# Kernel tuning notes

Measured on AMD Instinct MI355X. Metric: run time of the kernel, lower is better.

## Reference

```python
import jax, jax.numpy as jnp
import numpy as np

B = 2
S0, S1, S2 = 1024, 256, 64
S = S0 + S1 + S2
H, KV, D = 16, 8, 128
H_VLM, H_EXP = 2048, 1024
F_VLM, F_EXP = 8192, 4096
EPS = 1e-6
ROPE_BASE = 1000000.0


def setup_inputs() -> dict:
    key = jax.random.key(0)
    ks = iter(jax.random.split(key, 64))

    def n(shape, scale=0.02):
        return jax.random.normal(next(ks), shape, jnp.float32) * scale

    inp = {}
    inp["x0"] = jax.random.normal(next(ks), (B, S0, H_VLM), jnp.float32)
    inp["x1"] = jax.random.normal(next(ks), (B, S1, H_EXP), jnp.float32)
    inp["x2"] = jax.random.normal(next(ks), (B, S2, H_EXP), jnp.float32)
    inp["attention_mask"] = jnp.zeros((B, 1, S, S), jnp.float32)
    inp["position_ids"] = jnp.broadcast_to(jnp.arange(S, dtype=jnp.int32), (B, S))
    for i, (hid, ffn) in enumerate([(H_VLM, F_VLM), (H_EXP, F_EXP), (H_EXP, F_EXP)]):
        p = f"e{i}_"
        inp[p + "ln1"] = jnp.ones((hid,), jnp.float32)
        inp[p + "ln2"] = jnp.ones((hid,), jnp.float32)
        inp[p + "wq"] = n((H * D, hid))
        inp[p + "wk"] = n((KV * D, hid))
        inp[p + "wv"] = n((KV * D, hid))
        inp[p + "wo"] = n((hid, H * D))
        inp[p + "qn"] = jnp.ones((D,), jnp.float32)
        inp[p + "kn"] = jnp.ones((D,), jnp.float32)
        inp[p + "wg"] = n((ffn, hid))
        inp[p + "wu"] = n((ffn, hid))
        inp[p + "wd"] = n((hid, ffn))
    return inp


def _rms(x, w):
    # Qwen3 RMSNorm (eps 1e-6), applied over the last dim
    return x * jax.lax.rsqrt(jnp.mean(x * x, axis=-1, keepdims=True) + EPS) * w


def _rope_cos_sin(pos):
    inv = 1.0 / (ROPE_BASE ** (jnp.arange(0, D, 2, dtype=jnp.float32) / D))
    freqs = pos.astype(jnp.float32)[..., None] * inv  # [B,S,D/2]
    emb = jnp.concatenate([freqs, freqs], axis=-1)  # [B,S,D]
    return jnp.cos(emb), jnp.sin(emb)


def _rot_half(x):
    x1, x2 = jnp.split(x, 2, axis=-1)
    return jnp.concatenate([-x2, x1], axis=-1)


def _forward(xs, params, attention_mask, position_ids):
    # Per-expert QKV projections with per-head q/k RMSNorm
    qs, ks, vs = [], [], []
    for x, p in zip(xs, params):
        ln1, ln2, wq, wk, wv, wo, qn, kn, wg, wu, wd = p
        h = _rms(x, ln1)
        b, s, _ = x.shape
        q = _rms(jnp.einsum('bsd,od->bso', h, wq).reshape(b, s, H, D), qn)
        k = _rms(jnp.einsum('bsd,od->bso', h, wk).reshape(b, s, KV, D), kn)
        v = jnp.einsum('bsd,od->bso', h, wv).reshape(b, s, KV, D)
        qs.append(q.transpose(0, 2, 1, 3))  # [B,H,s,D]
        ks.append(k.transpose(0, 2, 1, 3))
        vs.append(v.transpose(0, 2, 1, 3))
    # Joint cross-expert attention over concatenated sequence
    q = jnp.concatenate(qs, axis=2)  # [B,H,S,D]
    k = jnp.concatenate(ks, axis=2)  # [B,KV,S,D]
    v = jnp.concatenate(vs, axis=2)
    cos, sin = _rope_cos_sin(position_ids)
    cos, sin = cos[:, None], sin[:, None]  # unsqueeze head dim
    q = q * cos + _rot_half(q) * sin
    k = k * cos + _rot_half(k) * sin
    k = jnp.repeat(k, H // KV, axis=1)  # GQA repeat_kv
    v = jnp.repeat(v, H // KV, axis=1)
    scores = jnp.einsum('bhqd,bhkd->bhqk', q, k) * (D ** -0.5) + attention_mask
    probs = jax.nn.softmax(scores, axis=-1)
    att = jnp.einsum('bhqk,bhkd->bhqd', probs, v)
    att = att.transpose(0, 2, 1, 3).reshape(q.shape[0], -1, H * D)  # [B,S,H*D]
    # Split back per expert: o_proj + residual + post-LN + SwiGLU MLP + residual
    outs, start = [], 0
    for x, p in zip(xs, params):
        ln1, ln2, wq, wk, wv, wo, qn, kn, wg, wu, wd = p
        s = x.shape[1]
        o = jnp.einsum('bsi,oi->bso', att[:, start:start + s], wo) + x
        h = _rms(o, ln2)
        m = jax.nn.silu(jnp.einsum('bsd,fd->bsf', h, wg)) * jnp.einsum('bsd,fd->bsf', h, wu)
        outs.append(jnp.einsum('bsf,df->bsd', m, wd) + o)
        start += s
    return tuple(outs)


def reference(x0, x1, x2, attention_mask, position_ids,
              e0_ln1, e0_ln2, e0_wq, e0_wk, e0_wv, e0_wo, e0_qn, e0_kn, e0_wg, e0_wu, e0_wd,
              e1_ln1, e1_ln2, e1_wq, e1_wk, e1_wv, e1_wo, e1_qn, e1_kn, e1_wg, e1_wu, e1_wd,
              e2_ln1, e2_ln2, e2_wq, e2_wk, e2_wv, e2_wo, e2_qn, e2_kn, e2_wg, e2_wu, e2_wd):
    params = [
        (e0_ln1, e0_ln2, e0_wq, e0_wk, e0_wv, e0_wo, e0_qn, e0_kn, e0_wg, e0_wu, e0_wd),
        (e1_ln1, e1_ln2, e1_wq, e1_wk, e1_wv, e1_wo, e1_qn, e1_kn, e1_wg, e1_wu, e1_wd),
        (e2_ln1, e2_ln2, e2_wq, e2_wk, e2_wv, e2_wo, e2_qn, e2_kn, e2_wg, e2_wu, e2_wd),
    ]
    return _forward([x0, x1, x2], params, attention_mask, position_ids)
```

## Files before the change

### kernel.cpp

```cpp
#include <hip/hip_runtime.h>
#include <cstdint>
#include <cstddef>


using u16 = unsigned short;
typedef __attribute__((ext_vector_type(4))) float  f32x4;
typedef __attribute__((ext_vector_type(4))) u16    u16x4;
typedef __attribute__((ext_vector_type(8))) u16    u16x8;
typedef __attribute__((ext_vector_type(8))) short  s16x8;

__device__ __forceinline__ u16 f2bf(float f) {
  unsigned u = __builtin_bit_cast(unsigned, f);
  u = (u + 0x7FFF + ((u >> 16) & 1)) >> 16;
  return (u16)u;
}
__device__ __forceinline__ float bf2f(u16 h) {
  unsigned u = ((unsigned)h) << 16;
  return __builtin_bit_cast(float, u);
}
__device__ __forceinline__ f32x4 mfma16(s16x8 a, s16x8 b, f32x4 c) {
  return __builtin_amdgcn_mfma_f32_16x16x32_bf16(a, b, c, 0, 0, 0);
}
__device__ __forceinline__ void gl_lds16(const u16* g, u16* l) {
  __builtin_amdgcn_global_load_lds(
      (const __attribute__((address_space(1))) unsigned int*)g,
      (__attribute__((address_space(3))) unsigned int*)l, 16, 0, 0);
}

static constexpr size_t WB_OFF   = 0;
static constexpr size_t H1_OFF   = WB_OFF   + 201326592;
static constexpr size_t H2_OFF   = H1_OFF   + 9699328;
static constexpr size_t QKV_OFF  = H2_OFF   + 9699328;
static constexpr size_t QB_OFF   = QKV_OFF  + 22020096;
static constexpr size_t KB_OFF   = QB_OFF   + 11010048;
static constexpr size_t VT_OFF   = KB_OFF   + 5505024;
static constexpr size_t ATTO_OFF = VT_OFF   + 5505024;
static constexpr size_t GU_OFF   = ATTO_OFF + 11010048;
static constexpr size_t WS_NEED  = GU_OFF   + 77594624;

struct CastTab { const float* src[15]; int pre[16]; };
struct DstoArg { size_t v[15]; };

__global__ __launch_bounds__(256) void cast_weights2(CastTab tab, DstoArg dsto,
                                                     u16* __restrict__ dst) {
  int c = blockIdx.x;
  int a = 0;
  while (c >= tab.pre[a + 1]) a++;
  const f32x4* s = (const f32x4*)(tab.src[a] + ((size_t)(c - tab.pre[a]) << 15));
  u16x4* d = (u16x4*)(dst + dsto.v[a] + (((size_t)(c - tab.pre[a])) << 15));
  int t = threadIdx.x;
  for (int i = t; i < 8192; i += 256) {
    f32x4 v = s[i];
    u16x4 o; o[0] = f2bf(v[0]); o[1] = f2bf(v[1]); o[2] = f2bf(v[2]); o[3] = f2bf(v[3]);
    d[i] = o;
  }
}

__global__ __launch_bounds__(256) void cast_gu_all(
    const float* __restrict__ g0, const float* __restrict__ u0,
    const float* __restrict__ g1, const float* __restrict__ u1,
    const float* __restrict__ g2, const float* __restrict__ u2,
    u16* __restrict__ dst, size_t o0, size_t o1, size_t o2) {
  const long N0 = 8388608, N1 = 10485760, N2 = 12582912;
  long i = (long)blockIdx.x * 256 + threadIdx.x;
  long stride = (long)gridDim.x * 256;
  for (; i < N2; i += stride) {
    const float* g; const float* u; u16* d; int logh; long li;
    if (i < N0)      { g = g0; u = u0; d = dst + o0; logh = 11; li = i; }
    else if (i < N1) { g = g1; u = u1; d = dst + o1; logh = 10; li = i - N0; }
    else             { g = g2; u = u2; d = dst + o2; logh = 10; li = i - N1; }
    int hid = 1 << logh;
    long e4 = li << 2;
    long r = e4 >> logh;
    int  k = (int)(e4 & (hid - 1));
    long super = r >> 6; int sub = (int)(r & 63);
    const float* src = (sub < 32 ? g + ((super << 5) + sub) * (long)hid
                                 : u + ((super << 5) + (sub - 32)) * (long)hid) + k;
    f32x4 v = *(const f32x4*)src;
    u16x4 o; o[0] = f2bf(v[0]); o[1] = f2bf(v[1]); o[2] = f2bf(v[2]); o[3] = f2bf(v[3]);
    ((u16x4*)d)[li] = o;
  }
}

__global__ __launch_bounds__(256) void rms_all(
    const float* __restrict__ i0, const float* __restrict__ i1, const float* __restrict__ i2,
    const float* __restrict__ w0, const float* __restrict__ w1, const float* __restrict__ w2,
    u16* __restrict__ out) {
  int row = blockIdx.x;
  const float* xr; const float* wr; size_t oo; int hid;
  if (row < 2048)      { xr = i0 + (size_t)row * 2048; wr = w0; oo = (size_t)row * 2048; hid = 2048; }
  else if (row < 2560) { int r = row - 2048; xr = i1 + (size_t)r * 1024; wr = w1;
                         oo = 4194304 + (size_t)r * 1024; hid = 1024; }
  else                 { int r = row - 2560; xr = i2 + (size_t)r * 1024; wr = w2;
                         oo = 4718592 + (size_t)r * 1024; hid = 1024; }
  const f32x4* x4 = (const f32x4*)xr;
  const f32x4* w4 = (const f32x4*)wr;
  int n4 = hid >> 2;
  int t = threadIdx.x;
  float ss = 0.f;
  for (int i = t; i < n4; i += 256) {
    f32x4 v = x4[i];
    ss += v[0] * v[0] + v[1] * v[1] + v[2] * v[2] + v[3] * v[3];
  }
#pragma unroll
  for (int m = 1; m < 64; m <<= 1) ss += __shfl_xor(ss, m);
  __shared__ float part[4];
  if ((t & 63) == 0) part[t >> 6] = ss;
  __syncthreads();
  float tot = part[0] + part[1] + part[2] + part[3];
  float rs = rsqrtf(tot / (float)hid + 1e-6f);
  u16x4* orow = (u16x4*)(out + oo);
  for (int i = t; i < n4; i += 256) {
    f32x4 v = x4[i];
    f32x4 g = w4[i];
    u16x4 o;
    o[0] = f2bf(v[0] * rs * g[0]); o[1] = f2bf(v[1] * rs * g[1]);
    o[2] = f2bf(v[2] * rs * g[2]); o[3] = f2bf(v[3] * rs * g[3]);
    orow[i] = o;
  }
}

template <int MB, int N0>
__device__ __forceinline__ void mmblk(f32x4 (&acc)[8][4], const s16x8 (&afr)[2][4],
                                      const s16x8 (&bfr)[2][4]) {
#pragma unroll
  for (int ks = 0; ks < 2; ks++)
#pragma unroll
    for (int j = 0; j < 4; j++)
#pragma unroll
      for (int ni = 0; ni < 2; ni++)
        acc[MB + j][N0 + ni] =
            mfma16(afr[ks][j], bfr[ks][N0 + ni], acc[MB + j][N0 + ni]);
}

#define GB256_BAR() do { __builtin_amdgcn_sched_barrier(0); \
                         __builtin_amdgcn_s_barrier(); } while (0)
#define GB256_LGKM0() do { asm volatile("s_waitcnt lgkmcnt(0)" ::: "memory"); \
                           __builtin_amdgcn_sched_barrier(0); } while (0)

template <int RESID, int OUTBF, bool SPLIT, bool SILU>
__global__ __launch_bounds__(512, 2) void gemm256(
    const u16* __restrict__ A, int Astride, int logSe, int bstride, int rowoff,
    const u16* __restrict__ Bw, int K, int kLen, int N,
    void* __restrict__ C, const float* __restrict__ R, size_t mn) {
  __shared__ u16 As[256 * 64];
  __shared__ u16 Bs[256 * 64];
  const int t = threadIdx.x;

  int gx = gridDim.x, nwg = gx * gridDim.y;
  int flat = blockIdx.y * gx + blockIdx.x;
  int q = nwg >> 3, r8 = nwg & 7;
  int xcd = flat & 7, idx = flat >> 3;
  int nf = (xcd < r8 ? xcd * (q + 1) : r8 * (q + 1) + (xcd - r8) * q) + idx;
  const int nt = (nf % gx) * 256, mt = (nf / gx) * 256;

  const int w = t >> 6, l = t & 63;
  const int wm = (w >> 2) * 128, wn = (w & 3) * 64;
  const int l15 = l & 15, lg = l >> 4;
  const int sr8 = t >> 3, u8 = t & 7;
  const int mask_se = (1 << logSe) - 1;
  const int k0 = SPLIT ? (int)blockIdx.z * kLen : 0;
  const int kLast = k0 + kLen - 64;

  f32x4 acc[8][4];
#pragma unroll
  for (int i = 0; i < 8; i++)
#pragma unroll
    for (int j = 0; j < 4; j++) acc[i][j] = (f32x4){0.f, 0.f, 0.f, 0.f};

  auto stA = [&](int qb, int ktv) {
    int row = qb + sr8;
    int gr = mt + row;
    int grow = ((gr >> logSe) * bstride) + (gr & mask_se) + rowoff;
    int su = u8 ^ (row & 7);
    gl_lds16(A + (size_t)grow * Astride + ktv + su * 8, &As[row * 64 + u8 * 8]);
  };
  auto stB = [&](int half, int pair, int ktv) {
    int row = (pair * 2 + (t >> 8)) * 64 + half * 32 + ((t & 255) >> 3);
    int su = u8 ^ (row & 7);
    gl_lds16(Bw + (size_t)(nt + row) * K + ktv + su * 8, &Bs[row * 64 + u8 * 8]);
  };
  auto rdA = [&](int mi, int ks) -> s16x8 {
    int row = wm + mi * 16 + l15;
    int u = ks * 4 + lg;
    return *(const s16x8*)&As[row * 64 + (u ^ (row & 7)) * 8];
  };
  auto rdB = [&](int ni, int ks) -> s16x8 {
    int row = wn + ni * 16 + l15;
    int u = ks * 4 + lg;
    return *(const s16x8*)&Bs[row * 64 + (u ^ (row & 7)) * 8];
  };

  stA(0, k0); stA(128, k0);
  stB(0, 0, k0); stB(0, 1, k0);
  stB(1, 0, k0); stB(1, 1, k0);
  stA(64, k0); stA(192, k0);
  asm volatile("s_waitcnt vmcnt(4)" ::: "memory");
  GB256_BAR();

  s16x8 afr[2][4], bfr[2][4];
  for (int kt0 = k0; kt0 < k0 + kLen; kt0 += 64) {
    int ktp = (kt0 + 64 <= kLast) ? kt0 + 64 : kLast;
#pragma unroll
    for (int ks = 0; ks < 2; ks++) {
#pragma unroll
      for (int j = 0; j < 4; j++) afr[ks][j] = rdA(j, ks);
#pragma unroll
      for (int j = 0; j < 2; j++) bfr[ks][j] = rdB(j, ks);
    }
    GB256_BAR();
    GB256_LGKM0();
    __builtin_amdgcn_s_setprio(1);
    mmblk<0, 0>(acc, afr, bfr);
    __builtin_amdgcn_s_setprio(0);
    asm volatile("s_waitcnt vmcnt(2)" ::: "memory");
    GB256_BAR();
#pragma unroll
    for (int ks = 0; ks < 2; ks++)
#pragma unroll
      for (int j = 2; j < 4; j++) bfr[ks][j] = rdB(j, ks);
    stA(0, ktp); stA(128, ktp);
    stB(0, 0, ktp); stB(0, 1, ktp);
    GB256_BAR();
    GB256_LGKM0();
    __builtin_amdgcn_s_setprio(1);
    mmblk<0, 2>(acc, afr, bfr);
    __builtin_amdgcn_s_setprio(0);
    asm volatile("s_waitcnt vmcnt(4)" ::: "memory");
    GB256_BAR();
#pragma unroll
    for (int ks = 0; ks < 2; ks++)
#pragma unroll
      for (int j = 0; j < 4; j++) afr[ks][j] = rdA(4 + j, ks);
    stB(1, 0, ktp); stB(1, 1, ktp);
    GB256_BAR();
    GB256_LGKM0();
    __builtin_amdgcn_s_setprio(1);
    mmblk<4, 0>(acc, afr, bfr);
    __builtin_amdgcn_s_setprio(0);
    GB256_BAR();
    stA(64, ktp); stA(192, ktp);
    __builtin_amdgcn_s_setprio(1);
    mmblk<4, 2>(acc, afr, bfr);
    __builtin_amdgcn_s_setprio(0);
    asm volatile("s_waitcnt vmcnt(4)" ::: "memory");
    GB256_BAR();
  }
  asm volatile("s_waitcnt vmcnt(0)" ::: "memory");

  float* Pz = SPLIT ? ((float*)C + (size_t)blockIdx.z * mn) : nullptr;
#pragma unroll
  for (int mi = 0; mi < 8; mi++) {
#pragma unroll
    for (int r = 0; r < 4; r++) {
      int crow = mt + wm + mi * 16 + lg * 4 + r;
      if (SILU) {
        size_t rb = (size_t)crow * (N >> 1);
        int super = (nt + wn) >> 6;
#pragma unroll
        for (int ni = 0; ni < 2; ni++) {
          int col = super * 32 + ni * 16 + l15;
          float g = acc[mi][ni][r], u = acc[mi][ni + 2][r];
          float s = g / (1.f + __expf(-g));
          ((u16*)C)[rb + col] = f2bf(s * u);
        }
      } else {
        size_t rb = (size_t)crow * N;
#pragma unroll
        for (int ni = 0; ni < 4; ni++) {
          int col = nt + wn + ni * 16 + l15;
          float v = acc[mi][ni][r];
          if (SPLIT) {
            Pz[rb + col] = v;
          } else {
            if (RESID == 1) v += R[rb + col];
            if (RESID == 2) v += ((const float*)C)[rb + col];
            if (OUTBF) ((u16*)C)[rb + col] = f2bf(v);
            else       ((float*)C)[rb + col] = v;
          }
        }
      }
    }
  }
}

struct GSeg {
  const u16* A; const u16* Bw; float* C;
  int Astride, logSe, bstride, rowoff;
  int K, kLen, N, nx, ntiles;
  size_t mn;
};
struct GJobs { GSeg s[2]; int cum[3]; };

__global__ __launch_bounds__(256) void gemm_jobs(GJobs J) {
  const int t = threadIdx.x;
  int flat = blockIdx.x;
  int si = (flat >= J.cum[1]) ? 1 : 0;
  const GSeg g = J.s[si];
  int local = flat - J.cum[si];
  int z = local / g.ntiles;
  int tl = local - z * g.ntiles;
  int count = g.ntiles;
  int q = count >> 3, r8 = count & 7;
  int xcd = tl & 7, idx = tl >> 3;
  int nf = (xcd < r8 ? xcd * (q + 1) : r8 * (q + 1) + (xcd - r8) * q) + idx;
  const int nt = nf % g.nx, mt = nf / g.nx;
  const int k0 = z * g.kLen;

  __shared__ u16 As[128 * 64];
  __shared__ u16 Bs[128 * 64];
  const int w = t >> 6, l = t & 63;
  const int wr = (w >> 1) * 64, wc = (w & 1) * 64;
  const int l15 = l & 15, lg = l >> 4;
  f32x4 acc[4][4];
#pragma unroll
  for (int i = 0; i < 4; i++)
#pragma unroll
    for (int j = 0; j < 4; j++) acc[i][j] = (f32x4){0.f, 0.f, 0.f, 0.f};

  const int sr = t >> 3, su0 = t & 7;
  const int mask_se = (1 << g.logSe) - 1;
  const int k1 = k0 + g.kLen;

  for (int kt = k0; kt < k1; kt += 64) {
    __syncthreads();
#pragma unroll
    for (int i = 0; i < 4; i++) {
      int row = i * 32 + sr;
      int gr = mt * 128 + row;
      int grow = ((gr >> g.logSe) * g.bstride) + (gr & mask_se) + g.rowoff;
      int su = su0 ^ (row & 7);
      gl_lds16(g.A + (size_t)grow * g.Astride + kt + su * 8, &As[row * 64 + su0 * 8]);
    }
#pragma unroll
    for (int i = 0; i < 4; i++) {
      int row = i * 32 + sr;
      int gc = nt * 128 + row;
      int su = su0 ^ (row & 7);
      gl_lds16(g.Bw + (size_t)gc * g.K + kt + su * 8, &Bs[row * 64 + su0 * 8]);
    }
    __syncthreads();

    s16x8 af[2][4], bfr[2][4];
#pragma unroll
    for (int mi = 0; mi < 4; mi++) {
      int row = wr + mi * 16 + l15;
#pragma unroll
      for (int ks = 0; ks < 2; ks++) {
        int u = ks * 4 + lg;
        af[ks][mi] = *(const s16x8*)&As[row * 64 + (u ^ (row & 7)) * 8];
      }
    }
#pragma unroll
    for (int ni = 0; ni < 4; ni++) {
      int row = wc + ni * 16 + l15;
#pragma unroll
      for (int ks = 0; ks < 2; ks++) {
        int u = ks * 4 + lg;
        bfr[ks][ni] = *(const s16x8*)&Bs[row * 64 + (u ^ (row & 7)) * 8];
      }
    }
#pragma unroll
    for (int ks = 0; ks < 2; ks++)
#pragma unroll
      for (int mi = 0; mi < 4; mi++)
#pragma unroll
        for (int ni = 0; ni < 4; ni++)
          acc[mi][ni] = mfma16(af[ks][mi], bfr[ks][ni], acc[mi][ni]);
  }

  float* Pz = g.C + (size_t)z * g.mn;
#pragma unroll
  for (int mi = 0; mi < 4; mi++) {
#pragma unroll
    for (int r = 0; r < 4; r++) {
      int crow = mt * 128 + wr + mi * 16 + lg * 4 + r;
      size_t rb = (size_t)crow * g.N;
#pragma unroll
      for (int ni = 0; ni < 4; ni++) {
        int col = nt * 128 + wc + ni * 16 + l15;
        Pz[rb + col] = acc[mi][ni][r];
      }
    }
  }
}

struct RSeg3 { const float* part; float* C; const float* R; int nz; size_t mn4; int nb; };
struct R3 { RSeg3 s[3]; };

template <int MODE>
__global__ __launch_bounds__(256) void reduce3(R3 J) {
  int b = blockIdx.x, si = 0, base = 0;
  while (si < 2 && b >= base + J.s[si].nb) { base += J.s[si].nb; si++; }
  RSeg3 g = J.s[si];
  const f32x4* p4 = (const f32x4*)g.part;
  for (size_t i = (size_t)(b - base) * 256 + threadIdx.x; i < g.mn4;
       i += (size_t)g.nb * 256) {
    f32x4 s = p4[i];
    for (int z = 1; z < g.nz; z++) s += p4[(size_t)z * g.mn4 + i];
    if (MODE == 1) s += ((const f32x4*)g.R)[i];
    else           s += ((const f32x4*)g.C)[i];
    ((f32x4*)g.C)[i] = s;
  }
}

struct RSegS { const float* part; u16* mout; int nz; size_t mnF4; int F4; size_t mnPart; int nb; };
struct RS2 { RSegS s[2]; };

__global__ __launch_bounds__(256) void reduce_silu2(RS2 J) {
  int b = blockIdx.x, si = 0, base = 0;
  if (b >= J.s[0].nb) { base = J.s[0].nb; si = 1; }
  RSegS g = J.s[si];
  for (size_t i = (size_t)(b - base) * 256 + threadIdx.x; i < g.mnF4;
       i += (size_t)g.nb * 256) {
    size_t row = i / g.F4;
    int cm4 = (int)(i - row * g.F4) * 4;
    int super = cm4 >> 5, j = cm4 & 31;
    size_t gb = row * (size_t)(g.F4 * 8) + (size_t)super * 64 + j;
    f32x4 gg = *(const f32x4*)(g.part + gb);
    f32x4 uu = *(const f32x4*)(g.part + gb + 32);
    for (int z = 1; z < g.nz; z++) {
      gg += *(const f32x4*)(g.part + (size_t)z * g.mnPart + gb);
      uu += *(const f32x4*)(g.part + (size_t)z * g.mnPart + gb + 32);
    }
    u16x4 o;
#pragma unroll
    for (int k = 0; k < 4; k++) {
      float s = gg[k] / (1.f + __expf(-gg[k]));
      o[k] = f2bf(s * uu[k]);
    }
    *(u16x4*)(g.mout + row * (size_t)(g.F4 * 4) + cm4) = o;
  }
}

__global__ __launch_bounds__(256) void qk_rope(
    const float* __restrict__ pe0, const float* __restrict__ pe1,
    const float* __restrict__ pe2,
    const float* __restrict__ qn0, const float* __restrict__ qn1, const float* __restrict__ qn2,
    const float* __restrict__ kn0, const float* __restrict__ kn1, const float* __restrict__ kn2,
    const int* __restrict__ pos, u16* __restrict__ Q, u16* __restrict__ K) {
  int tk = blockIdx.x;
  int b = tk / 1344, sg = tk % 1344;
  int w = threadIdx.x >> 6, l = threadIdx.x & 63;
  int hr = blockIdx.y * 4 + w;
  int e, off, Se;
  if (sg < 1024)      { e = 0; off = 0;    Se = 1024; }
  else if (sg < 1280) { e = 1; off = 1024; Se = 256;  }
  else                { e = 2; off = 1280; Se = 64;   }
  int r = b * Se + (sg - off);
  const float* P; size_t mn; int nz;
  if (e == 0)      { P = pe0; mn = 8388608; nz = 2; }
  else if (e == 1) { P = pe1; mn = 2097152; nz = 2; }
  else             { P = pe2; mn = 524288;  nz = 4; }
  size_t base = (size_t)r * 4096;
  int c0; const float* nw; u16* dst;
  if (hr < 16) {
    c0 = hr * 128 + l;
    nw = (e == 0) ? qn0 : (e == 1) ? qn1 : qn2;
    dst = Q + ((size_t)(b * 16 + hr) * 1344 + sg) * 128;
  } else {
    int kh = hr - 16;
    c0 = 2048 + kh * 128 + l;
    nw = (e == 0) ? kn0 : (e == 1) ? kn1 : kn2;
    dst = K + ((size_t)(b * 8 + kh) * 1344 + sg) * 128;
  }
  float x0v = 0.f, x1v = 0.f;
  for (int z = 0; z < nz; z++) {
    const float* pz = P + (size_t)z * mn + base;
    x0v += pz[c0];
    x1v += pz[c0 + 64];
  }
  float ss = x0v * x0v + x1v * x1v;
#pragma unroll
  for (int m = 1; m < 64; m <<= 1) ss += __shfl_xor(ss, m);
  float rs = rsqrtf(ss * (1.f / 128.f) + 1e-6f);
  float y0 = x0v * rs * nw[l], y1 = x1v * rs * nw[l + 64];
  float p = (float)pos[b * 1344 + sg];
  float inv = exp2f(-(float)l * 0.3114307588956902f);
  float th = p * inv;
  float cz = __cosf(th), sz = __sinf(th);
  dst[l]      = f2bf(y0 * cz - y1 * sz);
  dst[l + 64] = f2bf(y1 * cz + y0 * sz);
}

__global__ __launch_bounds__(256) void v_trans(
    const float* __restrict__ pe0, const float* __restrict__ pe1,
    const float* __restrict__ pe2, u16* __restrict__ Vt) {
  __shared__ u16 tile[64][72];
  int st = blockIdx.x;
  int b = st / 21, s0 = (st % 21) * 64;
  int kvh = blockIdx.y >> 1, dh = (blockIdx.y & 1) * 64;
  int t = threadIdx.x;
  int sl = t >> 2, d0 = (t & 3) * 16;
  int sg = s0 + sl;
  int e, off, Se;
  if (sg < 1024)      { e = 0; off = 0;    Se = 1024; }
  else if (sg < 1280) { e = 1; off = 1024; Se = 256;  }
  else                { e = 2; off = 1280; Se = 64;   }
  int r = b * Se + (sg - off);
  const float* P; size_t mn; int nz;
  if (e == 0)      { P = pe0; mn = 8388608; nz = 2; }
  else if (e == 1) { P = pe1; mn = 2097152; nz = 2; }
  else             { P = pe2; mn = 524288;  nz = 4; }
  size_t base = (size_t)r * 4096 + 3072 + kvh * 128 + dh + d0;
  float a16[16];
#pragma unroll
  for (int j = 0; j < 16; j++) a16[j] = 0.f;
  for (int z = 0; z < nz; z++) {
    const f32x4* p4 = (const f32x4*)(P + (size_t)z * mn + base);
#pragma unroll
    for (int q4 = 0; q4 < 4; q4++) {
      f32x4 v = p4[q4];
      a16[q4 * 4 + 0] += v[0]; a16[q4 * 4 + 1] += v[1];
      a16[q4 * 4 + 2] += v[2]; a16[q4 * 4 + 3] += v[3];
    }
  }
#pragma unroll
  for (int j = 0; j < 16; j++) tile[sl][d0 + j] = f2bf(a16[j]);
  __syncthreads();
  int dl = t >> 2, sb = (t & 3) * 16;
  u16* dst = Vt + ((size_t)(b * 8 + kvh) * 128 + dh + dl) * 1344 + s0 + sb;
  u16x8 o0, o1;
#pragma unroll
  for (int j = 0; j < 8; j++) { o0[j] = tile[sb + j][dl]; o1[j] = tile[sb + 8 + j][dl]; }
  *(u16x8*)dst = o0;
  *(u16x8*)(dst + 8) = o1;
}

__global__ __launch_bounds__(256, 3) void attn(
    const u16* __restrict__ Q, const u16* __restrict__ K, const u16* __restrict__ Vt,
    u16* __restrict__ attO) {
  constexpr int S = 1344;
  __shared__ u16 Qs[64 * 128];
  __shared__ u16 Ks[64 * 128];
  __shared__ u16 Vts[128 * 64];
  u16 (*Ps)[16 * 64] = (u16 (*)[16 * 64])Qs;
  int bh = blockIdx.y;
  int b = bh >> 4, h = bh & 15, kvh = h >> 1;
  int q0 = blockIdx.x * 64;
  int t = threadIdx.x, w = t >> 6, l = t & 63;
  const int l15 = l & 15, lg = l >> 4;
  const u16* Qg = Q + ((size_t)(b * 16 + h) * S + q0) * 128;
  const u16* Kg = K + ((size_t)(b * 8 + kvh) * S) * 128;
  const u16* Vg = Vt + ((size_t)(b * 8 + kvh) * 128) * S;

  {
    int unit = t & 15, r16 = t >> 4;
#pragma unroll
    for (int i = 0; i < 4; i++) {
      int row = i * 16 + r16;
      int su = (unit & 8) | ((unit & 7) ^ (row & 7));
      gl_lds16(Qg + (size_t)row * 128 + su * 8, &Qs[row * 128 + unit * 8]);
    }
  }
  __syncthreads();
  s16x8 qf[4];
  {
    int qrow = w * 16 + l15;
#pragma unroll
    for (int ks = 0; ks < 4; ks++) {
      int u = ks * 4 + lg;
      int su = (u & 8) | ((u & 7) ^ (qrow & 7));
      qf[ks] = *(const s16x8*)&Qs[qrow * 128 + su * 8];
    }
  }

  float mrow[4] = {-3e38f, -3e38f, -3e38f, -3e38f};
  float lrow[4] = {0.f, 0.f, 0.f, 0.f};
  f32x4 of[8];
#pragma unroll
  for (int d = 0; d < 8; d++) of[d] = (f32x4){0.f, 0.f, 0.f, 0.f};
  const float scale = 0.08838834764831845f;

  for (int kt = 0; kt < 21; ++kt) {
    int k0 = kt * 64;
    __syncthreads();
    {
      int unit = t & 15, r16 = t >> 4;
#pragma unroll
      for (int i = 0; i < 4; i++) {
        int row = i * 16 + r16;
        int su = (unit & 8) | ((unit & 7) ^ (row & 7));
        gl_lds16(Kg + (size_t)(k0 + row) * 128 + su * 8, &Ks[row * 128 + unit * 8]);
      }
      int u8 = t & 7, r32 = t >> 3;
#pragma unroll
      for (int i = 0; i < 4; i++) {
        int row = i * 32 + r32;
        int su = u8 ^ (row & 7);
        gl_lds16(Vg + (size_t)row * S + k0 + su * 8, &Vts[row * 64 + u8 * 8]);
      }
    }
    __syncthreads();

    f32x4 sf[4];
    __builtin_amdgcn_s_setprio(1);
#pragma unroll
    for (int cb = 0; cb < 4; cb++) {
      f32x4 a = (f32x4){0.f, 0.f, 0.f, 0.f};
      int krow = cb * 16 + l15;
#pragma unroll
      for (int ks = 0; ks < 4; ks++) {
        int u = ks * 4 + lg;
        int su = (u & 8) | ((u & 7) ^ (krow & 7));
        s16x8 kf = *(const s16x8*)&Ks[krow * 128 + su * 8];
        a = mfma16(qf[ks], kf, a);
      }
      sf[cb] = a;
    }
    __builtin_amdgcn_s_setprio(0);

    float pv[4][4], tmax[4];
#pragma unroll
    for (int r = 0; r < 4; r++) {
      float v0 = sf[0][r] * scale;
      float v1 = sf[1][r] * scale;
      float v2 = sf[2][r] * scale;
      float v3 = sf[3][r] * scale;
      pv[0][r] = v0; pv[1][r] = v1; pv[2][r] = v2; pv[3][r] = v3;
      tmax[r] = fmaxf(fmaxf(v0, v1), fmaxf(v2, v3));
    }
#pragma unroll
    for (int m = 1; m < 16; m <<= 1)
#pragma unroll
      for (int r = 0; r < 4; r++) tmax[r] = fmaxf(tmax[r], __shfl_xor(tmax[r], m));

    int need = 0;
#pragma unroll
    for (int r = 0; r < 4; r++) need |= (tmax[r] > mrow[r] + 8.f) ? 1 : 0;
    if (__any(need)) {
      float fr[4];
#pragma unroll
      for (int r = 0; r < 4; r++) {
        float mnew = fmaxf(mrow[r], tmax[r]);
        fr[r] = __expf(mrow[r] - mnew);
        mrow[r] = mnew;
        lrow[r] *= fr[r];
      }
#pragma unroll
      for (int d = 0; d < 8; d++)
#pragma unroll
        for (int r = 0; r < 4; r++) of[d][r] *= fr[r];
    }
#pragma unroll
    for (int r = 0; r < 4; r++) {
      float rs = 0.f;
#pragma unroll
      for (int cb = 0; cb < 4; cb++) { pv[cb][r] = __expf(pv[cb][r] - mrow[r]); rs += pv[cb][r]; }
#pragma unroll
      for (int m = 1; m < 16; m <<= 1) rs += __shfl_xor(rs, m);
      lrow[r] += rs;
    }

#pragma unroll
    for (int cb = 0; cb < 4; cb++)
#pragma unroll
      for (int r = 0; r < 4; r++) {
        int prow = lg * 4 + r;
        int col = cb * 16 + l15;
        int su = (col >> 3) ^ (prow & 7);
        Ps[w][prow * 64 + su * 8 + (col & 7)] = f2bf(pv[cb][r]);
      }
    __syncthreads();

    s16x8 pa[2];
#pragma unroll
    for (int ks = 0; ks < 2; ks++) {
      int prow = l15;
      int u = ks * 4 + lg;
      pa[ks] = *(const s16x8*)&Ps[w][prow * 64 + (u ^ (prow & 7)) * 8];
    }
    __builtin_amdgcn_s_setprio(1);
#pragma unroll
    for (int d = 0; d < 8; d++) {
      int vrow = d * 16 + l15;
#pragma unroll
      for (int ks = 0; ks < 2; ks++) {
        int u = ks * 4 + lg;
        s16x8 vf = *(const s16x8*)&Vts[vrow * 64 + (u ^ (vrow & 7)) * 8];
        of[d] = mfma16(pa[ks], vf, of[d]);
      }
    }
    __builtin_amdgcn_s_setprio(0);
  }

#pragma unroll
  for (int r = 0; r < 4; r++) {
    float il = 1.f / lrow[r];
    int sg = q0 + w * 16 + lg * 4 + r;
    u16* orow = attO + ((size_t)(b * S + sg)) * 2048 + h * 128;
#pragma unroll
    for (int d = 0; d < 8; d++) orow[d * 16 + l15] = f2bf(of[d][r] * il);
  }
}

extern "C" void kernel_launch(void* const* d_in, const int* in_sizes, int n_in,
                              void* d_out, int out_size, void* d_ws, size_t ws_size,
                              hipStream_t stream) {
  if (ws_size < WS_NEED) return;

  const float* x[3] = {(const float*)d_in[0], (const float*)d_in[1], (const float*)d_in[2]};
  const int* pos = (const int*)d_in[4];
  auto W = [&](int e, int k) -> const float* { return (const float*)d_in[5 + e * 11 + k]; };

  char* ws = (char*)d_ws;
  u16* wbf  = (u16*)(ws + WB_OFF);
  u16* h1   = (u16*)(ws + H1_OFF);
  u16* h2   = (u16*)(ws + H2_OFF);
  u16* Qb   = (u16*)(ws + QB_OFF);
  u16* Kb   = (u16*)(ws + KB_OFF);
  u16* Vtb  = (u16*)(ws + VT_OFF);
  u16* attO = (u16*)(ws + ATTO_OFF);
  u16* m    = (u16*)(ws + GU_OFF);
  float* scrA = (float*)(ws + GU_OFF);
  float* scrC = (float*)(ws + H1_OFF);
  float* dout = (float*)d_out;

  const int hid[3] = {2048, 1024, 1024}, ffn[3] = {8192, 4096, 4096};
  const size_t douto[3] = {0, 4194304, 4718592};
  const size_t mo[3]    = {0, 16777216, 18874368};

  size_t woff[3][7];
  CastTab tab;
  DstoArg dsarg;
  {
    size_t cum = 0; int cc = 0, ci = 0;
    for (int e = 0; e < 3; e++) {
      const size_t sz[7] = {(size_t)2048 * hid[e], (size_t)1024 * hid[e], (size_t)1024 * hid[e],
                            (size_t)2048 * hid[e], (size_t)ffn[e] * hid[e],
                            (size_t)ffn[e] * hid[e], (size_t)ffn[e] * hid[e]};
      const int kidx[7] = {2, 3, 4, 5, 8, 9, 10};
      for (int j = 0; j < 7; j++) {
        woff[e][j] = cum;
        if (j != 4 && j != 5) {
          tab.src[ci] = W(e, kidx[j]);
          tab.pre[ci] = cc;
          dsarg.v[ci] = cum;
          cc += (int)(sz[j] >> 15);
          ci++;
        }
        cum += sz[j];
      }
    }
    tab.pre[15] = cc;
  }

  cast_weights2<<<dim3(1536), dim3(256), 0, stream>>>(tab, dsarg, wbf);
  cast_gu_all<<<dim3(2048), dim3(256), 0, stream>>>(
      W(0, 8), W(0, 9), W(1, 8), W(1, 9), W(2, 8), W(2, 9),
      wbf, woff[0][4], woff[1][4], woff[2][4]);

  rms_all<<<dim3(2688), dim3(256), 0, stream>>>(
      x[0], x[1], x[2], W(0, 0), W(1, 0), W(2, 0), h1);

  float* qp1 = (float*)(ws + QKV_OFF);
  float* qp2 = (float*)(ws + H2_OFF);
  gemm256<0, 0, true, false><<<dim3(16, 8, 2), dim3(512), 0, stream>>>(
      h1, 2048, 11, 0, 0, wbf + woff[0][0], 2048, 1024, 4096, scrA, nullptr,
      (size_t)8388608);
  {
    GJobs J = {};
    J.s[0] = {h1 + douto[1], wbf + woff[1][0], qp1, 1024, 9, 0, 0,
              1024, 512, 4096, 32, 128, (size_t)2097152};
    J.s[1] = {h1 + douto[2], wbf + woff[2][0], qp2, 1024, 7, 0, 0,
              1024, 256, 4096, 32, 32, (size_t)524288};
    J.cum[0] = 0; J.cum[1] = 256; J.cum[2] = 384;
    gemm_jobs<<<dim3(384), dim3(256), 0, stream>>>(J);
  }

  qk_rope<<<dim3(2688, 6), dim3(256), 0, stream>>>(
      scrA, qp1, qp2, W(0, 6), W(1, 6), W(2, 6), W(0, 7), W(1, 7), W(2, 7),
      pos, Qb, Kb);
  v_trans<<<dim3(42, 16), dim3(256), 0, stream>>>(scrA, qp1, qp2, Vtb);

  attn<<<dim3(21, 32), dim3(256), 0, stream>>>(Qb, Kb, Vtb, attO);

  gemm256<0, 0, true, false><<<dim3(8, 8, 4), dim3(512), 0, stream>>>(
      attO, 2048, 10, 1344, 0, wbf + woff[0][3], 2048, 512, 2048, scrA, nullptr,
      (size_t)4194304);
  {
    float* p1 = (float*)(ws + QKV_OFF);
    float* p2 = (float*)(ws + QKV_OFF + 16777216);
    GJobs J = {};
    J.s[0] = {attO, wbf + woff[1][3], p1, 2048, 8, 1344, 1024,
              2048, 256, 1024, 8, 32, (size_t)524288};
    J.s[1] = {attO, wbf + woff[2][3], p2, 2048, 6, 1344, 1280,
              2048, 128, 1024, 8, 8, (size_t)131072};
    J.cum[0] = 0; J.cum[1] = 256; J.cum[2] = 384;
    gemm_jobs<<<dim3(384), dim3(256), 0, stream>>>(J);
    R3 R = {};
    R.s[0] = {scrA, dout, x[0], 4, 1048576, 1536};
    R.s[1] = {p1, dout + douto[1], x[1], 8, 131072, 192};
    R.s[2] = {p2, dout + douto[2], x[2], 16, 32768, 48};
    reduce3<1><<<dim3(1776), dim3(256), 0, stream>>>(R);
  }

  rms_all<<<dim3(2688), dim3(256), 0, stream>>>(
      dout, dout + douto[1], dout + douto[2], W(0, 1), W(1, 1), W(2, 1), h2);

  gemm256<0, 0, false, true><<<dim3(64, 8), dim3(512), 0, stream>>>(
      h2, 2048, 11, 0, 0, wbf + woff[0][4], 2048, 2048, 16384, m, nullptr, 0);
  {
    float* p1 = (float*)(ws + QKV_OFF);
    float* p2 = (float*)(ws + QKV_OFF + 33554432);
    GJobs J = {};
    J.s[0] = {h2 + douto[1], wbf + woff[1][4], p1, 1024, 9, 0, 0,
              1024, 512, 8192, 64, 256, (size_t)4194304};
    J.s[1] = {h2 + douto[2], wbf + woff[2][4], p2, 1024, 7, 0, 0,
              1024, 256, 8192, 64, 64, (size_t)1048576};
    J.cum[0] = 0; J.cum[1] = 512; J.cum[2] = 768;
    gemm_jobs<<<dim3(768), dim3(256), 0, stream>>>(J);
    RS2 R = {};
    R.s[0] = {p1, m + mo[1], 2, 524288, 1024, 4194304, 2048};
    R.s[1] = {p2, m + mo[2], 4, 131072, 1024, 1048576, 512};
    reduce_silu2<<<dim3(2560), dim3(256), 0, stream>>>(R);
  }

  gemm256<0, 0, true, false><<<dim3(8, 8, 4), dim3(512), 0, stream>>>(
      m, 8192, 11, 0, 0, wbf + woff[0][6], 8192, 2048, 2048, scrC, nullptr,
      (size_t)4194304);
  {
    float* p1 = (float*)(ws + GU_OFF + 38797312);
    float* p2 = (float*)(ws + GU_OFF + 38797312 + 16777216);
    GJobs J = {};
    J.s[0] = {m + mo[1], wbf + woff[1][6], p1, 4096, 9, 0, 0,
              4096, 512, 1024, 8, 32, (size_t)524288};
    J.s[1] = {m + mo[2], wbf + woff[2][6], p2, 4096, 7, 0, 0,
              4096, 256, 1024, 8, 8, (size_t)131072};
    J.cum[0] = 0; J.cum[1] = 256; J.cum[2] = 384;
    gemm_jobs<<<dim3(384), dim3(256), 0, stream>>>(J);
    R3 R = {};
    R.s[0] = {scrC, dout, nullptr, 4, 1048576, 1536};
    R.s[1] = {p1, dout + douto[1], nullptr, 8, 131072, 192};
    R.s[2] = {p2, dout + douto[2], nullptr, 16, 32768, 48};
    reduce3<2><<<dim3(1776), dim3(256), 0, stream>>>(R);
  }
}
```

Before: 690.1 us.

## Merge per-expert GEMMs into one segmented 256-tile kernel launch

Replaces the separate expert-0 gemm256 launch and the 128-tile gemm_jobs launch for experts 1 and 2 with a single segmented gemm256_seg kernel that covers all three experts. The small experts now run on 256x256 tiles with a row-validity guard. Their split-K factors change: fewer splits, and none for the QKV projection. The SwiGLU gate/up product is fused into the epilogue for all experts, so the reduce_silu2 pass and its partial buffers go away. This cuts launches and partial-sum traffic, but small experts waste compute on padded 256-row tiles and have fewer blocks in flight.

```diff
diff --git a/kernel.cpp b/kernel.cpp
--- a/kernel.cpp
+++ b/kernel.cpp
@@ -120,6 +120,14 @@
   }
 }
 
+struct S256 {
+  const u16* A; const u16* Bw; void* C;
+  int Astride, logSe, bstride, rowoff;
+  int K, kLen, N, nx, ntiles, mode, Mvalid;
+  size_t zmn;
+};
+struct J256 { S256 s[3]; int cum[4]; int nseg; };
+
 template <int MB, int N0>
 __device__ __forceinline__ void mmblk(f32x4 (&acc)[8][4], const s16x8 (&afr)[2][4],
                                       const s16x8 (&bfr)[2][4]) {
@@ -138,29 +146,31 @@
 #define GB256_LGKM0() do { asm volatile("s_waitcnt lgkmcnt(0)" ::: "memory"); \
                            __builtin_amdgcn_sched_barrier(0); } while (0)
 
-template <int RESID, int OUTBF, bool SPLIT, bool SILU>
-__global__ __launch_bounds__(512, 2) void gemm256(
-    const u16* __restrict__ A, int Astride, int logSe, int bstride, int rowoff,
-    const u16* __restrict__ Bw, int K, int kLen, int N,
-    void* __restrict__ C, const float* __restrict__ R, size_t mn) {
+__global__ __launch_bounds__(512, 2) void gemm256_seg(J256 J) {
+  const int t = threadIdx.x;
+  int flat = blockIdx.x;
+  int si = 0;
+  while (si + 1 < J.nseg && flat >= J.cum[si + 1]) si++;
+  const S256 g = J.s[si];
+  int local = flat - J.cum[si];
+  int z = local / g.ntiles;
+  int tl = local - z * g.ntiles;
+
+  int count = g.ntiles;
+  int q = count >> 3, r8 = count & 7;
+  int xcd = tl & 7, idx = tl >> 3;
+  int nf = (xcd < r8 ? xcd * (q + 1) : r8 * (q + 1) + (xcd - r8) * q) + idx;
+  const int nt = (nf % g.nx) * 256, mt = (nf / g.nx) * 256;
+
   __shared__ u16 As[256 * 64];
   __shared__ u16 Bs[256 * 64];
-  const int t = threadIdx.x;
-
-  int gx = gridDim.x, nwg = gx * gridDim.y;
-  int flat = blockIdx.y * gx + blockIdx.x;
-  int q = nwg >> 3, r8 = nwg & 7;
-  int xcd = flat & 7, idx = flat >> 3;
-  int nf = (xcd < r8 ? xcd * (q + 1) : r8 * (q + 1) + (xcd - r8) * q) + idx;
-  const int nt = (nf % gx) * 256, mt = (nf / gx) * 256;
-
   const int w = t >> 6, l = t & 63;
   const int wm = (w >> 2) * 128, wn = (w & 3) * 64;
   const int l15 = l & 15, lg = l >> 4;
   const int sr8 = t >> 3, u8 = t & 7;
-  const int mask_se = (1 << logSe) - 1;
-  const int k0 = SPLIT ? (int)blockIdx.z * kLen : 0;
-  const int kLast = k0 + kLen - 64;
+  const int mask_se = (1 << g.logSe) - 1;
+  const int k0 = z * g.kLen;
+  const int kLast = k0 + g.kLen - 64;
 
   f32x4 acc[8][4];
 #pragma unroll
@@ -171,14 +181,14 @@
   auto stA = [&](int qb, int ktv) {
     int row = qb + sr8;
     int gr = mt + row;
-    int grow = ((gr >> logSe) * bstride) + (gr & mask_se) + rowoff;
+    int grow = ((gr >> g.logSe) * g.bstride) + (gr & mask_se) + g.rowoff;
     int su = u8 ^ (row & 7);
-    gl_lds16(A + (size_t)grow * Astride + ktv + su * 8, &As[row * 64 + u8 * 8]);
+    gl_lds16(g.A + (size_t)grow * g.Astride + ktv + su * 8, &As[row * 64 + u8 * 8]);
   };
   auto stB = [&](int half, int pair, int ktv) {
     int row = (pair * 2 + (t >> 8)) * 64 + half * 32 + ((t & 255) >> 3);
     int su = u8 ^ (row & 7);
-    gl_lds16(Bw + (size_t)(nt + row) * K + ktv + su * 8, &Bs[row * 64 + u8 * 8]);
+    gl_lds16(g.Bw + (size_t)(nt + row) * g.K + ktv + su * 8, &Bs[row * 64 + u8 * 8]);
   };
   auto rdA = [&](int mi, int ks) -> s16x8 {
     int row = wm + mi * 16 + l15;
@@ -199,7 +209,7 @@
   GB256_BAR();
 
   s16x8 afr[2][4], bfr[2][4];
-  for (int kt0 = k0; kt0 < k0 + kLen; kt0 += 64) {
+  for (int kt0 = k0; kt0 < k0 + g.kLen; kt0 += 64) {
     int ktp = (kt0 + 64 <= kLast) ? kt0 + 64 : kLast;
 #pragma unroll
     for (int ks = 0; ks < 2; ks++) {
@@ -248,138 +258,30 @@
   }
   asm volatile("s_waitcnt vmcnt(0)" ::: "memory");
 
-  float* Pz = SPLIT ? ((float*)C + (size_t)blockIdx.z * mn) : nullptr;
+  float* Pz = (float*)g.C + (size_t)z * g.zmn;
 #pragma unroll
   for (int mi = 0; mi < 8; mi++) {
 #pragma unroll
     for (int r = 0; r < 4; r++) {
       int crow = mt + wm + mi * 16 + lg * 4 + r;
-      if (SILU) {
-        size_t rb = (size_t)crow * (N >> 1);
+      if (crow >= g.Mvalid) continue;
+      if (g.mode == 4) {
+        size_t rb = (size_t)crow * (g.N >> 1);
         int super = (nt + wn) >> 6;
 #pragma unroll
         for (int ni = 0; ni < 2; ni++) {
           int col = super * 32 + ni * 16 + l15;
-          float g = acc[mi][ni][r], u = acc[mi][ni + 2][r];
-          float s = g / (1.f + __expf(-g));
-          ((u16*)C)[rb + col] = f2bf(s * u);
+          float gg = acc[mi][ni][r], uu = acc[mi][ni + 2][r];
+          float s = gg / (1.f + __expf(-gg));
+          ((u16*)g.C)[rb + col] = f2bf(s * uu);
         }
       } else {
-        size_t rb = (size_t)crow * N;
+        size_t rb = (size_t)crow * g.N;
 #pragma unroll
         for (int ni = 0; ni < 4; ni++) {
           int col = nt + wn + ni * 16 + l15;
-          float v = acc[mi][ni][r];
-          if (SPLIT) {
-            Pz[rb + col] = v;
-          } else {
-            if (RESID == 1) v += R[rb + col];
-            if (RESID == 2) v += ((const float*)C)[rb + col];
-            if (OUTBF) ((u16*)C)[rb + col] = f2bf(v);
-            else       ((float*)C)[rb + col] = v;
-          }
+          Pz[rb + col] = acc[mi][ni][r];
         }
-      }
-    }
-  }
-}
-
-struct GSeg {
-  const u16* A; const u16* Bw; float* C;
-  int Astride, logSe, bstride, rowoff;
-  int K, kLen, N, nx, ntiles;
-  size_t mn;
-};
-struct GJobs { GSeg s[2]; int cum[3]; };
-
-__global__ __launch_bounds__(256) void gemm_jobs(GJobs J) {
-  const int t = threadIdx.x;
-  int flat = blockIdx.x;
-  int si = (flat >= J.cum[1]) ? 1 : 0;
-  const GSeg g = J.s[si];
-  int local = flat - J.cum[si];
-  int z = local / g.ntiles;
-  int tl = local - z * g.ntiles;
-  int count = g.ntiles;
-  int q = count >> 3, r8 = count & 7;
-  int xcd = tl & 7, idx = tl >> 3;
-  int nf = (xcd < r8 ? xcd * (q + 1) : r8 * (q + 1) + (xcd - r8) * q) + idx;
-  const int nt = nf % g.nx, mt = nf / g.nx;
-  const int k0 = z * g.kLen;
-
-  __shared__ u16 As[128 * 64];
-  __shared__ u16 Bs[128 * 64];
-  const int w = t >> 6, l = t & 63;
-  const int wr = (w >> 1) * 64, wc = (w & 1) * 64;
-  const int l15 = l & 15, lg = l >> 4;
-  f32x4 acc[4][4];
-#pragma unroll
-  for (int i = 0; i < 4; i++)
-#pragma unroll
-    for (int j = 0; j < 4; j++) acc[i][j] = (f32x4){0.f, 0.f, 0.f, 0.f};
-
-  const int sr = t >> 3, su0 = t & 7;
-  const int mask_se = (1 << g.logSe) - 1;
-  const int k1 = k0 + g.kLen;
-
-  for (int kt = k0; kt < k1; kt += 64) {
-    __syncthreads();
-#pragma unroll
-    for (int i = 0; i < 4; i++) {
-      int row = i * 32 + sr;
-      int gr = mt * 128 + row;
-      int grow = ((gr >> g.logSe) * g.bstride) + (gr & mask_se) + g.rowoff;
-      int su = su0 ^ (row & 7);
-      gl_lds16(g.A + (size_t)grow * g.Astride + kt + su * 8, &As[row * 64 + su0 * 8]);
-    }
-#pragma unroll
-    for (int i = 0; i < 4; i++) {
-      int row = i * 32 + sr;
-      int gc = nt * 128 + row;
-      int su = su0 ^ (row & 7);
-      gl_lds16(g.Bw + (size_t)gc * g.K + kt + su * 8, &Bs[row * 64 + su0 * 8]);
-    }
-    __syncthreads();
-
-    s16x8 af[2][4], bfr[2][4];
-#pragma unroll
-    for (int mi = 0; mi < 4; mi++) {
-      int row = wr + mi * 16 + l15;
-#pragma unroll
-      for (int ks = 0; ks < 2; ks++) {
-        int u = ks * 4 + lg;
-        af[ks][mi] = *(const s16x8*)&As[row * 64 + (u ^ (row & 7)) * 8];
-      }
-    }
-#pragma unroll
-    for (int ni = 0; ni < 4; ni++) {
-      int row = wc + ni * 16 + l15;
-#pragma unroll
-      for (int ks = 0; ks < 2; ks++) {
-        int u = ks * 4 + lg;
-        bfr[ks][ni] = *(const s16x8*)&Bs[row * 64 + (u ^ (row & 7)) * 8];
-      }
-    }
-#pragma unroll
-    for (int ks = 0; ks < 2; ks++)
-#pragma unroll
-      for (int mi = 0; mi < 4; mi++)
-#pragma unroll
-        for (int ni = 0; ni < 4; ni++)
-          acc[mi][ni] = mfma16(af[ks][mi], bfr[ks][ni], acc[mi][ni]);
-  }
-
-  float* Pz = g.C + (size_t)z * g.mn;
-#pragma unroll
-  for (int mi = 0; mi < 4; mi++) {
-#pragma unroll
-    for (int r = 0; r < 4; r++) {
-      int crow = mt * 128 + wr + mi * 16 + lg * 4 + r;
-      size_t rb = (size_t)crow * g.N;
-#pragma unroll
-      for (int ni = 0; ni < 4; ni++) {
-        int col = nt * 128 + wc + ni * 16 + l15;
-        Pz[rb + col] = acc[mi][ni][r];
       }
     }
   }
@@ -401,35 +303,6 @@
     if (MODE == 1) s += ((const f32x4*)g.R)[i];
     else           s += ((const f32x4*)g.C)[i];
     ((f32x4*)g.C)[i] = s;
-  }
-}
-
-struct RSegS { const float* part; u16* mout; int nz; size_t mnF4; int F4; size_t mnPart; int nb; };
-struct RS2 { RSegS s[2]; };
-
-__global__ __launch_bounds__(256) void reduce_silu2(RS2 J) {
-  int b = blockIdx.x, si = 0, base = 0;
-  if (b >= J.s[0].nb) { base = J.s[0].nb; si = 1; }
-  RSegS g = J.s[si];
-  for (size_t i = (size_t)(b - base) * 256 + threadIdx.x; i < g.mnF4;
-       i += (size_t)g.nb * 256) {
-    size_t row = i / g.F4;
-    int cm4 = (int)(i - row * g.F4) * 4;
-    int super = cm4 >> 5, j = cm4 & 31;
-    size_t gb = row * (size_t)(g.F4 * 8) + (size_t)super * 64 + j;
-    f32x4 gg = *(const f32x4*)(g.part + gb);
-    f32x4 uu = *(const f32x4*)(g.part + gb + 32);
-    for (int z = 1; z < g.nz; z++) {
-      gg += *(const f32x4*)(g.part + (size_t)z * g.mnPart + gb);
-      uu += *(const f32x4*)(g.part + (size_t)z * g.mnPart + gb + 32);
-    }
-    u16x4 o;
-#pragma unroll
-    for (int k = 0; k < 4; k++) {
-      float s = gg[k] / (1.f + __expf(-gg[k]));
-      o[k] = f2bf(s * uu[k]);
-    }
-    *(u16x4*)(g.mout + row * (size_t)(g.F4 * 4) + cm4) = o;
   }
 }
 
@@ -450,8 +323,8 @@
   int r = b * Se + (sg - off);
   const float* P; size_t mn; int nz;
   if (e == 0)      { P = pe0; mn = 8388608; nz = 2; }
-  else if (e == 1) { P = pe1; mn = 2097152; nz = 2; }
-  else             { P = pe2; mn = 524288;  nz = 4; }
+  else if (e == 1) { P = pe1; mn = 0; nz = 1; }
+  else             { P = pe2; mn = 0; nz = 1; }
   size_t base = (size_t)r * 4096;
   int c0; const float* nw; u16* dst;
   if (hr < 16) {
@@ -500,8 +373,8 @@
   int r = b * Se + (sg - off);
   const float* P; size_t mn; int nz;
   if (e == 0)      { P = pe0; mn = 8388608; nz = 2; }
-  else if (e == 1) { P = pe1; mn = 2097152; nz = 2; }
-  else             { P = pe2; mn = 524288;  nz = 4; }
+  else if (e == 1) { P = pe1; mn = 0; nz = 1; }
+  else             { P = pe2; mn = 0; nz = 1; }
   size_t base = (size_t)r * 4096 + 3072 + kvh * 128 + dh + d0;
   float a16[16];
 #pragma unroll
@@ -755,17 +628,17 @@
 
   float* qp1 = (float*)(ws + QKV_OFF);
   float* qp2 = (float*)(ws + H2_OFF);
-  gemm256<0, 0, true, false><<<dim3(16, 8, 2), dim3(512), 0, stream>>>(
-      h1, 2048, 11, 0, 0, wbf + woff[0][0], 2048, 1024, 4096, scrA, nullptr,
-      (size_t)8388608);
   {
-    GJobs J = {};
-    J.s[0] = {h1 + douto[1], wbf + woff[1][0], qp1, 1024, 9, 0, 0,
-              1024, 512, 4096, 32, 128, (size_t)2097152};
-    J.s[1] = {h1 + douto[2], wbf + woff[2][0], qp2, 1024, 7, 0, 0,
-              1024, 256, 4096, 32, 32, (size_t)524288};
-    J.cum[0] = 0; J.cum[1] = 256; J.cum[2] = 384;
-    gemm_jobs<<<dim3(384), dim3(256), 0, stream>>>(J);
+    J256 J = {};
+    J.s[0] = {h1, wbf + woff[0][0], scrA, 2048, 11, 0, 0,
+              2048, 1024, 4096, 16, 128, 0, 2048, (size_t)8388608};
+    J.s[1] = {h1 + douto[1], wbf + woff[1][0], qp1, 1024, 9, 0, 0,
+              1024, 1024, 4096, 16, 32, 0, 512, 0};
+    J.s[2] = {h1 + douto[2], wbf + woff[2][0], qp2, 1024, 7, 0, 0,
+              1024, 1024, 4096, 16, 16, 0, 128, 0};
+    J.cum[0] = 0; J.cum[1] = 256; J.cum[2] = 288; J.cum[3] = 304;
+    J.nseg = 3;
+    gemm256_seg<<<dim3(304), dim3(512), 0, stream>>>(J);
   }
 
   qk_rope<<<dim3(2688, 6), dim3(256), 0, stream>>>(
@@ -775,64 +648,59 @@
 
   attn<<<dim3(21, 32), dim3(256), 0, stream>>>(Qb, Kb, Vtb, attO);
 
-  gemm256<0, 0, true, false><<<dim3(8, 8, 4), dim3(512), 0, stream>>>(
-      attO, 2048, 10, 1344, 0, wbf + woff[0][3], 2048, 512, 2048, scrA, nullptr,
-      (size_t)4194304);
   {
     float* p1 = (float*)(ws + QKV_OFF);
     float* p2 = (float*)(ws + QKV_OFF + 16777216);
-    GJobs J = {};
-    J.s[0] = {attO, wbf + woff[1][3], p1, 2048, 8, 1344, 1024,
-              2048, 256, 1024, 8, 32, (size_t)524288};
-    J.s[1] = {attO, wbf + woff[2][3], p2, 2048, 6, 1344, 1280,
-              2048, 128, 1024, 8, 8, (size_t)131072};
-    J.cum[0] = 0; J.cum[1] = 256; J.cum[2] = 384;
-    gemm_jobs<<<dim3(384), dim3(256), 0, stream>>>(J);
+    J256 J = {};
+    J.s[0] = {attO, wbf + woff[0][3], scrA, 2048, 10, 1344, 0,
+              2048, 512, 2048, 8, 64, 0, 2048, (size_t)4194304};
+    J.s[1] = {attO, wbf + woff[1][3], p1, 2048, 8, 1344, 1024,
+              2048, 512, 1024, 4, 8, 0, 512, (size_t)524288};
+    J.s[2] = {attO, wbf + woff[2][3], p2, 2048, 6, 1344, 1280,
+              2048, 512, 1024, 4, 4, 0, 128, (size_t)131072};
+    J.cum[0] = 0; J.cum[1] = 256; J.cum[2] = 288; J.cum[3] = 304;
+    J.nseg = 3;
+    gemm256_seg<<<dim3(304), dim3(512), 0, stream>>>(J);
     R3 R = {};
     R.s[0] = {scrA, dout, x[0], 4, 1048576, 1536};
-    R.s[1] = {p1, dout + douto[1], x[1], 8, 131072, 192};
-    R.s[2] = {p2, dout + douto[2], x[2], 16, 32768, 48};
+    R.s[1] = {p1, dout + douto[1], x[1], 4, 131072, 192};
+    R.s[2] = {p2, dout + douto[2], x[2], 4, 32768, 48};
     reduce3<1><<<dim3(1776), dim3(256), 0, stream>>>(R);
   }
 
   rms_all<<<dim3(2688), dim3(256), 0, stream>>>(
       dout, dout + douto[1], dout + douto[2], W(0, 1), W(1, 1), W(2, 1), h2);
 
-  gemm256<0, 0, false, true><<<dim3(64, 8), dim3(512), 0, stream>>>(
-      h2, 2048, 11, 0, 0, wbf + woff[0][4], 2048, 2048, 16384, m, nullptr, 0);
   {
-    float* p1 = (float*)(ws + QKV_OFF);
-    float* p2 = (float*)(ws + QKV_OFF + 33554432);
-    GJobs J = {};
-    J.s[0] = {h2 + douto[1], wbf + woff[1][4], p1, 1024, 9, 0, 0,
-              1024, 512, 8192, 64, 256, (size_t)4194304};
-    J.s[1] = {h2 + douto[2], wbf + woff[2][4], p2, 1024, 7, 0, 0,
-              1024, 256, 8192, 64, 64, (size_t)1048576};
-    J.cum[0] = 0; J.cum[1] = 512; J.cum[2] = 768;
-    gemm_jobs<<<dim3(768), dim3(256), 0, stream>>>(J);
-    RS2 R = {};
-    R.s[0] = {p1, m + mo[1], 2, 524288, 1024, 4194304, 2048};
-    R.s[1] = {p2, m + mo[2], 4, 131072, 1024, 1048576, 512};
-    reduce_silu2<<<dim3(2560), dim3(256), 0, stream>>>(R);
-  }
-
-  gemm256<0, 0, true, false><<<dim3(8, 8, 4), dim3(512), 0, stream>>>(
-      m, 8192, 11, 0, 0, wbf + woff[0][6], 8192, 2048, 2048, scrC, nullptr,
-      (size_t)4194304);
+    J256 J = {};
+    J.s[0] = {h2, wbf + woff[0][4], m, 2048, 11, 0, 0,
+              2048, 2048, 16384, 64, 512, 4, 2048, 0};
+    J.s[1] = {h2 + douto[1], wbf + woff[1][4], m + mo[1], 1024, 9, 0, 0,
+              1024, 1024, 8192, 32, 64, 4, 512, 0};
+    J.s[2] = {h2 + douto[2], wbf + woff[2][4], m + mo[2], 1024, 7, 0, 0,
+              1024, 1024, 8192, 32, 32, 4, 128, 0};
+    J.cum[0] = 0; J.cum[1] = 512; J.cum[2] = 576; J.cum[3] = 608;
+    J.nseg = 3;
+    gemm256_seg<<<dim3(608), dim3(512), 0, stream>>>(J);
+  }
+
   {
     float* p1 = (float*)(ws + GU_OFF + 38797312);
     float* p2 = (float*)(ws + GU_OFF + 38797312 + 16777216);
-    GJobs J = {};
-    J.s[0] = {m + mo[1], wbf + woff[1][6], p1, 4096, 9, 0, 0,
-              4096, 512, 1024, 8, 32, (size_t)524288};
-    J.s[1] = {m + mo[2], wbf + woff[2][6], p2, 4096, 7, 0, 0,
-              4096, 256, 1024, 8, 8, (size_t)131072};
-    J.cum[0] = 0; J.cum[1] = 256; J.cum[2] = 384;
-    gemm_jobs<<<dim3(384), dim3(256), 0, stream>>>(J);
+    J256 J = {};
+    J.s[0] = {m, wbf + woff[0][6], scrC, 8192, 11, 0, 0,
+              8192, 2048, 2048, 8, 64, 0, 2048, (size_t)4194304};
+    J.s[1] = {m + mo[1], wbf + woff[1][6], p1, 4096, 9, 0, 0,
+              4096, 2048, 1024, 4, 8, 0, 512, (size_t)524288};
+    J.s[2] = {m + mo[2], wbf + woff[2][6], p2, 4096, 7, 0, 0,
+              4096, 2048, 1024, 4, 4, 0, 128, (size_t)131072};
+    J.cum[0] = 0; J.cum[1] = 256; J.cum[2] = 272; J.cum[3] = 280;
+    J.nseg = 3;
+    gemm256_seg<<<dim3(280), dim3(512), 0, stream>>>(J);
     R3 R = {};
     R.s[0] = {scrC, dout, nullptr, 4, 1048576, 1536};
-    R.s[1] = {p1, dout + douto[1], nullptr, 8, 131072, 192};
-    R.s[2] = {p2, dout + douto[2], nullptr, 16, 32768, 48};
+    R.s[1] = {p1, dout + douto[1], nullptr, 2, 131072, 192};
+    R.s[2] = {p2, dout + douto[2], nullptr, 2, 32768, 48};
     reduce3<2><<<dim3(1776), dim3(256), 0, stream>>>(R);
   }
 }
```

New measurement: 763.5 us. 1.11x slower.
